# Kernel optimization log

Measured on AMD Instinct MI355X. Metric: run time of the kernel, lower is better.

## Reference

```python
import jax, jax.numpy as jnp
import numpy as np

K = 3  # kernel_size
K2 = K * K


def _unfold_nhwc(x):
    """x: [B,H,W,C] -> patches [B,H,W,K2,C], k index = i*K+j (matches F.unfold ordering
    after the module's reshape to (B,C,k2,H,W))."""
    B, H, W, C = x.shape
    xp = jnp.pad(x, ((0, 0), (1, 1), (1, 1), (0, 0)))  # padding=1
    patches = jnp.stack(
        [xp[:, i:i + H, j:j + W, :] for i in range(K) for j in range(K)], axis=3
    )  # [B,H,W,K2,C]
    return patches


def setup_inputs() -> dict:
    key = jax.random.key(0)
    k1, k2, k3 = jax.random.split(key, 3)
    B, H, W, C = 8, 64, 64, 256
    x = jax.random.normal(k1, (B, H, W, C), dtype=jnp.float32)
    v_w = jax.random.normal(k2, (C, C), dtype=jnp.float32) * 0.02
    proj_w = jax.random.normal(k3, (C, C), dtype=jnp.float32) * 0.02
    proj_b = jnp.zeros((C,), dtype=jnp.float32)
    return {"x": x, "v_w": v_w, "proj_w": proj_w, "proj_b": proj_b}


def reference(x, v_w, proj_w, proj_b):
    # patches: [B,H,W,K2,C]
    patches = _unfold_nhwc(x)
    # v projection (Linear, no bias): [B,H,W,K2,D]
    v = jnp.einsum("bhwkc,dc->bhwkd", patches, v_w)
    # attn = softmax(eye(k2)); output is sliced to row 0 in the original,
    # so only the first row of the constant attention matrix matters.
    attn = jax.nn.softmax(jnp.eye(K2, dtype=v.dtype), axis=-1)  # [K2,K2]
    a0 = attn[0]  # [K2]
    out = jnp.einsum("bhwkd,k->bhwd", v, a0)  # == (attn @ v)[:, 0]
    # proj Linear with bias
    out = jnp.einsum("bhwd,ed->bhwe", out, proj_w) + proj_b
    return out
```

## Files before the change

kernel.cpp:

```cpp
#include <hip/hip_runtime.h>

typedef __attribute__((ext_vector_type(8))) short short8;
typedef __attribute__((ext_vector_type(4))) float f32x4;

__device__ __forceinline__ unsigned short f2bf(float f) {
    union { float f; unsigned int u; } v; v.f = f;
    unsigned int u = v.u;
    unsigned int r = u + 0x7FFFu + ((u >> 16) & 1u);
    return (unsigned short)(r >> 16);
}

__global__ __launch_bounds__(1024) void wmat_kernel(
    const float* __restrict__ v_w, const float* __restrict__ proj_w,
    unsigned short* __restrict__ Wm)
{
    __shared__ float red[4][256];
    const int e  = blockIdx.x;
    const int c  = threadIdx.x & 255;
    const int dq = threadIdx.x >> 8;

    const float* pw = proj_w + e * 256 + dq * 64;
    const float* vv = v_w + (dq * 64) * 256 + c;

    float acc = 0.f;
#pragma unroll 8
    for (int d = 0; d < 64; ++d)
        acc = fmaf(pw[d], vv[d * 256], acc);

    red[dq][c] = acc;
    __syncthreads();
    if (threadIdx.x < 256) {
        float s = red[0][c] + red[1][c] + red[2][c] + red[3][c];
        const int wn = e >> 6, ni = (e >> 4) & 3, lrow = e & 15;
        const int kk = c >> 5, lkg = (c >> 3) & 3, c8 = c & 7;
        const int lane = lkg * 16 + lrow;
        const int idxo = ((((wn * 8 + kk) * 4 + ni) * 64 + lane) * 8) + c8;
        Wm[idxo] = f2bf(s);
    }
}

__global__ __launch_bounds__(256, 8) void fused_kernel(
    const float* __restrict__ x, const unsigned short* __restrict__ Wm,
    const float* __restrict__ proj_b, float* __restrict__ out)
{
    const int idx   = ((blockIdx.x & 7) << 8) | (blockIdx.x >> 3);
    const int b     = idx >> 8;
    const int h     = (idx >> 2) & 63;
    const int wbase = (idx & 3) * 16;
    const int t     = threadIdx.x;

    __shared__ char ldsraw[16 * 256 * 4];

    const float A1  = (float)(1.0 / 10.71828182845904523536);
    const float A0D = (float)(2.71828182845904523536 / 10.71828182845904523536) - A1;

    {
        const int strip = t >> 5;
        const int c0    = (t & 31) * 8;
        const int px0   = strip * 2;
        const int gw0   = wbase + px0;

        const f32x4 z = {0.f, 0.f, 0.f, 0.f};
        f32x4 acc[2][2];
#pragma unroll
        for (int i = 0; i < 2; ++i) { acc[i][0] = z; acc[i][1] = z; }

        for (int r = h - 1; r <= h + 1; ++r) {
            if (r < 0 || r >= 64) continue;
            const bool top = (r == h - 1);
            const float* xr = x + (((size_t)b * 64 + r) * 64) * 256 + c0;

            f32x4 pm0, pm1, pc0, pc1;
            if (gw0 == 0) { pm0 = z; pm1 = z; }
            else {
                pm0 = *(const f32x4*)(xr + (gw0 - 1) * 256);
                pm1 = *(const f32x4*)(xr + (gw0 - 1) * 256 + 4);
            }
            pc0 = *(const f32x4*)(xr + gw0 * 256);
            pc1 = *(const f32x4*)(xr + gw0 * 256 + 4);

#pragma unroll
            for (int i = 0; i < 2; ++i) {
                const int gwn = gw0 + i + 1;
                f32x4 pn0 = z, pn1 = z;
                if (gwn < 64) {
                    pn0 = *(const f32x4*)(xr + gwn * 256);
                    pn1 = *(const f32x4*)(xr + gwn * 256 + 4);
                }
                acc[i][0] += A1 * (pm0 + pc0 + pn0);
                acc[i][1] += A1 * (pm1 + pc1 + pn1);
                if (top) {
                    acc[i][0] += A0D * pm0;
                    acc[i][1] += A0D * pm1;
                }
                pm0 = pc0; pm1 = pc1; pc0 = pn0; pc1 = pn1;
            }
        }

#pragma unroll
        for (int i = 0; i < 2; ++i) {
            const int w = px0 + i;
            union { short8 v; unsigned short u[8]; } pk;
#pragma unroll
            for (int j = 0; j < 4; ++j) {
                pk.u[j]     = f2bf(acc[i][0][j]);
                pk.u[4 + j] = f2bf(acc[i][1][j]);
            }
            unsigned baddr = ((unsigned)w * 512u + (unsigned)c0 * 2u) ^ (((unsigned)(w & 7)) << 4);
            *reinterpret_cast<short8*>(ldsraw + baddr) = pk.v;
        }
    }
    __syncthreads();

    const int wn   = t >> 6;
    const int lane = t & 63;
    const int lrow = lane & 15;
    const int lkg  = lane >> 4;

    f32x4 acc2[4];
    {
        const f32x4 z = {0.f, 0.f, 0.f, 0.f};
#pragma unroll
        for (int ni = 0; ni < 4; ++ni) acc2[ni] = z;

        const unsigned abase = (unsigned)lrow * 512u;
        const unsigned aswz  = ((unsigned)(lrow & 7)) << 4;
        const unsigned short* wv = Wm + (wn << 14) + (lane << 3);

#pragma unroll
        for (int kk = 0; kk < 8; ++kk) {
            const unsigned abyte = (abase + (unsigned)(kk * 64 + lkg * 16)) ^ aswz;
            short8 a = *reinterpret_cast<const short8*>(ldsraw + abyte);
            const unsigned short* wk = wv + (kk << 11);
#pragma unroll
            for (int ni = 0; ni < 4; ++ni) {
                short8 bf = *reinterpret_cast<const short8*>(wk + (ni << 9));
                acc2[ni] = __builtin_amdgcn_mfma_f32_16x16x32_bf16(bf, a, acc2[ni], 0, 0, 0);
            }
        }
    }
    __syncthreads();

#pragma unroll
    for (int ni = 0; ni < 4; ++ni) {
        unsigned baddr = ((unsigned)lrow * 1024u
                          + (unsigned)((wn * 64 + ni * 16 + lkg * 4) * 4))
                         ^ (((unsigned)(lrow & 7)) << 4);
        *reinterpret_cast<f32x4*>(ldsraw + baddr) = acc2[ni];
    }
    __syncthreads();

    const f32x4 bias = *reinterpret_cast<const f32x4*>(proj_b + lane * 4);
    const size_t pxbase = (size_t)idx * 16;
#pragma unroll
    for (int j = 0; j < 4; ++j) {
        const int row = j * 4 + wn;
        unsigned baddr = ((unsigned)row * 1024u + (unsigned)lane * 16u)
                         ^ (((unsigned)(row & 7)) << 4);
        f32x4 v = *reinterpret_cast<const f32x4*>(ldsraw + baddr) + bias;
        __builtin_nontemporal_store(v, reinterpret_cast<f32x4*>(out + (pxbase + row) * 256 + lane * 4));
    }
}

extern "C" void kernel_launch(void* const* d_in, const int* in_sizes, int n_in,
                              void* d_out, int out_size, void* d_ws, size_t ws_size,
                              hipStream_t stream) {
    const float* x      = (const float*)d_in[0];
    const float* v_w    = (const float*)d_in[1];
    const float* proj_w = (const float*)d_in[2];
    const float* proj_b = (const float*)d_in[3];
    float* out = (float*)d_out;
    unsigned short* Wm = (unsigned short*)d_ws;

    wmat_kernel<<<256, 1024, 0, stream>>>(v_w, proj_w, Wm);
    fused_kernel<<<2048, 256, 0, stream>>>(x, Wm, proj_b, out);
}
```

Baseline: 29.84 us.

## Double pixel tile per block and stage weight slices in LDS via global_load_lds

Each block now handles 32 pixels with 512 threads instead of 16 pixels with 256, so every weight slice fetched is reused across two MFMA row tiles. Weight fragments are copied into shared memory per k-step with direct global-to-LDS loads rather than read by each wave straight from global memory. This cuts global weight traffic per output but adds two block-wide barriers per k-step and doubles the LDS footprint, which can lower occupancy.

```diff
diff --git a/kernel.cpp b/kernel.cpp
--- a/kernel.cpp
+++ b/kernel.cpp
@@ -39,17 +39,17 @@
     }
 }
 
-__global__ __launch_bounds__(256, 8) void fused_kernel(
+__global__ __launch_bounds__(512, 8) void fused_kernel(
     const float* __restrict__ x, const unsigned short* __restrict__ Wm,
     const float* __restrict__ proj_b, float* __restrict__ out)
 {
-    const int idx   = ((blockIdx.x & 7) << 8) | (blockIdx.x >> 3);
-    const int b     = idx >> 8;
-    const int h     = (idx >> 2) & 63;
-    const int wbase = (idx & 3) * 16;
+    const int idx   = ((blockIdx.x & 7) << 7) | (blockIdx.x >> 3);
+    const int b     = idx >> 7;
+    const int h     = (idx >> 1) & 63;
+    const int wbase = (idx & 1) * 32;
     const int t     = threadIdx.x;
 
-    __shared__ char ldsraw[16 * 256 * 4];
+    __shared__ char lds[32768];
 
     const float A1  = (float)(1.0 / 10.71828182845904523536);
     const float A0D = (float)(2.71828182845904523536 / 10.71828182845904523536) - A1;
@@ -107,58 +107,67 @@
                 pk.u[4 + j] = f2bf(acc[i][1][j]);
             }
             unsigned baddr = ((unsigned)w * 512u + (unsigned)c0 * 2u) ^ (((unsigned)(w & 7)) << 4);
-            *reinterpret_cast<short8*>(ldsraw + baddr) = pk.v;
+            *reinterpret_cast<short8*>(lds + baddr) = pk.v;
         }
     }
-    __syncthreads();
 
-    const int wn   = t >> 6;
+    const int w    = t >> 6;
     const int lane = t & 63;
+    const int mi   = w >> 2;
+    const int wn   = w & 3;
     const int lrow = lane & 15;
     const int lkg  = lane >> 4;
+    const int row  = mi * 16 + lrow;
 
     f32x4 acc2[4];
     {
         const f32x4 z = {0.f, 0.f, 0.f, 0.f};
 #pragma unroll
         for (int ni = 0; ni < 4; ++ni) acc2[ni] = z;
+    }
 
-        const unsigned abase = (unsigned)lrow * 512u;
-        const unsigned aswz  = ((unsigned)(lrow & 7)) << 4;
-        const unsigned short* wv = Wm + (wn << 14) + (lane << 3);
+    const unsigned abase = (unsigned)row * 512u;
+    const unsigned aswz  = ((unsigned)(row & 7)) << 4;
 
+    for (int kk = 0; kk < 8; ++kk) {
+        __syncthreads();
 #pragma unroll
-        for (int kk = 0; kk < 8; ++kk) {
-            const unsigned abyte = (abase + (unsigned)(kk * 64 + lkg * 16)) ^ aswz;
-            short8 a = *reinterpret_cast<const short8*>(ldsraw + abyte);
-            const unsigned short* wk = wv + (kk << 11);
+        for (int q = 0; q < 2; ++q) {
+            const int g = w * 2 + q;
+            const unsigned short* src =
+                Wm + ((((size_t)(g >> 2) * 8 + kk) * 4 + (g & 3)) * 64 + lane) * 8;
+            __builtin_amdgcn_global_load_lds(src, (lds + 16384 + g * 1024), 16, 0, 0);
+        }
+        __syncthreads();
+
+        const unsigned abyte = (abase + (unsigned)(kk * 64 + lkg * 16)) ^ aswz;
+        short8 a = *reinterpret_cast<const short8*>(lds + abyte);
 #pragma unroll
-            for (int ni = 0; ni < 4; ++ni) {
-                short8 bf = *reinterpret_cast<const short8*>(wk + (ni << 9));
-                acc2[ni] = __builtin_amdgcn_mfma_f32_16x16x32_bf16(bf, a, acc2[ni], 0, 0, 0);
-            }
+        for (int ni = 0; ni < 4; ++ni) {
+            short8 bf = *reinterpret_cast<const short8*>(
+                lds + 16384 + ((wn * 4 + ni) * 64 + lane) * 16);
+            acc2[ni] = __builtin_amdgcn_mfma_f32_16x16x32_bf16(bf, a, acc2[ni], 0, 0, 0);
         }
     }
     __syncthreads();
 
 #pragma unroll
     for (int ni = 0; ni < 4; ++ni) {
-        unsigned baddr = ((unsigned)lrow * 1024u
-                          + (unsigned)((wn * 64 + ni * 16 + lkg * 4) * 4))
-                         ^ (((unsigned)(lrow & 7)) << 4);
-        *reinterpret_cast<f32x4*>(ldsraw + baddr) = acc2[ni];
+        const unsigned e0 = (unsigned)(wn * 64 + ni * 16 + lkg * 4);
+        unsigned baddr = ((unsigned)row * 1024u + e0 * 4u) ^ (((unsigned)(row & 7)) << 4);
+        *reinterpret_cast<f32x4*>(lds + baddr) = acc2[ni];
     }
     __syncthreads();
 
     const f32x4 bias = *reinterpret_cast<const f32x4*>(proj_b + lane * 4);
-    const size_t pxbase = (size_t)idx * 16;
+    const size_t pxbase = (size_t)idx * 32;
 #pragma unroll
     for (int j = 0; j < 4; ++j) {
-        const int row = j * 4 + wn;
-        unsigned baddr = ((unsigned)row * 1024u + (unsigned)lane * 16u)
-                         ^ (((unsigned)(row & 7)) << 4);
-        f32x4 v = *reinterpret_cast<const f32x4*>(ldsraw + baddr) + bias;
-        __builtin_nontemporal_store(v, reinterpret_cast<f32x4*>(out + (pxbase + row) * 256 + lane * 4));
+        const int r = j * 8 + w;
+        unsigned baddr = ((unsigned)r * 1024u + (unsigned)lane * 16u)
+                         ^ (((unsigned)(r & 7)) << 4);
+        f32x4 v = *reinterpret_cast<const f32x4*>(lds + baddr) + bias;
+        __builtin_nontemporal_store(v, reinterpret_cast<f32x4*>(out + (pxbase + r) * 256 + lane * 4));
     }
 }
 
@@ -173,5 +182,5 @@
     unsigned short* Wm = (unsigned short*)d_ws;
 
     wmat_kernel<<<256, 1024, 0, stream>>>(v_w, proj_w, Wm);
-    fused_kernel<<<2048, 256, 0, stream>>>(x, Wm, proj_b, out);
+    fused_kernel<<<1024, 512, 0, stream>>>(x, Wm, proj_b, out);
 }
```

Result: faster. 27.82 us (-6.8%).
